# Performance work log

Measured on AMD Instinct MI355X. Metric: run time of the kernel, lower is better.

## Reference

```python
import jax, jax.numpy as jnp
import numpy as np
from jax import lax

K = 50            # n_segments in original SLIC call
ITERS = 10        # SLIC k-means iterations (skimage default max_num_iter=10)
COMPACTNESS = 10.0  # skimage SLIC default compactness


def _slic_weights(img):
    """SLIC-style superpixel segmentation of img [H,W,3] -> per-pixel weight 1/|segment|.

    Faithful to the module's use of skimage.slic: k-means in joint (color, xy)
    space with spatial coords scaled by compactness/S, S = sqrt(H*W/K),
    grid-initialized centers, then weight[p] = 1/count(segment[p]).
    """
    H, W, _ = img.shape
    N = H * W
    S = float(np.sqrt(N / K))
    ratio = COMPACTNESS / S
    yy, xx = jnp.meshgrid(jnp.arange(H, dtype=img.dtype),
                          jnp.arange(W, dtype=img.dtype), indexing='ij')
    feats = jnp.concatenate(
        [img.reshape(N, 3), (jnp.stack([yy, xx], -1).reshape(N, 2)) * ratio],
        axis=-1)  # [N,5]

    # grid-initialized centers (static shapes -> numpy at trace time)
    n = int(np.ceil(np.sqrt(K)))
    cy = ((np.arange(n) + 0.5) * H / n).astype(np.int64)
    cx = ((np.arange(n) + 0.5) * W / n).astype(np.int64)
    gy, gx = np.meshgrid(cy, cx, indexing='ij')
    init_idx = jnp.asarray((gy * W + gx).reshape(-1)[:K])
    centers0 = feats[init_idx]  # [K,5]

    f2 = jnp.sum(feats * feats, axis=-1)  # [N]

    def assign(centers):
        # squared distances via expansion: avoids [N,K,5] intermediate
        c2 = jnp.sum(centers * centers, axis=-1)            # [K]
        d = f2[:, None] + c2[None, :] - 2.0 * feats @ centers.T  # [N,K]
        return jnp.argmin(d, axis=1)

    def step(centers, _):
        lab = assign(centers)
        sums = jax.ops.segment_sum(feats, lab, num_segments=K)
        cnts = jax.ops.segment_sum(jnp.ones((N,), feats.dtype), lab, num_segments=K)
        new_centers = sums / jnp.maximum(cnts, 1.0)[:, None]
        return new_centers, None

    centers, _ = lax.scan(step, centers0, None, length=ITERS)
    lab = assign(centers)                                   # [N]
    cnts = jax.ops.segment_sum(jnp.ones((N,), feats.dtype), lab, num_segments=K)
    w = (1.0 / jnp.maximum(cnts, 1.0))[lab]                 # [N], 1/|segment|
    return w.reshape(H, W)


def setup_inputs() -> dict:
    key = jax.random.key(0)
    x = jax.random.uniform(key, (16, 3, 512, 512), dtype=jnp.float32)
    return {"x": x}


def reference(x):
    # per-pixel segment weights (computed from detached data in the original)
    w = lax.stop_gradient(jax.vmap(_slic_weights)(x.transpose(0, 2, 3, 1)))  # [B,H,W]
    xw = x * w[:, None, :, :]                    # broadcast over RGB channels
    mean_rgb = jnp.mean(xw, axis=(2, 3), keepdims=True)  # [B,3,1,1]
    mr = mean_rgb[:, 0:1]
    mg = mean_rgb[:, 1:2]
    mb = mean_rgb[:, 2:3]
    Drg = (mr - mg) ** 2
    Drb = (mr - mb) ** 2
    Dgb = (mb - mg) ** 2
    k = jnp.sqrt(Drg ** 2 + Drb ** 2 + Dgb ** 2)  # [B,1,1,1]
    return k
```

## Files before the change

### kernel.cpp

```cpp
#include <hip/hip_runtime.h>
#include <cmath>

#define K_SEG 50
#define ITERS 10
#define NPASS (ITERS + 1)
#define H_IMG 512
#define W_IMG 512
#define NPIX (H_IMG * W_IMG)
#define BATCH 16
#define SLOTS (K_SEG * 6)
#define TOTAL_SLOTS (NPASS * BATCH * SLOTS)


__global__ void zero_all(double* __restrict__ g) {
    int i = blockIdx.x * 256 + threadIdx.x;
    if (i < TOTAL_SLOTS) g[i] = 0.0;
}

__global__ void __launch_bounds__(256) assign_fused(
        const float* __restrict__ x, double* __restrict__ gsums,
        int it, float ratiof) {
    __shared__ float cen[K_SEG][6];
    __shared__ float cmax[K_SEG];
    __shared__ double part[K_SEG][6];
    __shared__ int klist4[4][52];
    __shared__ int ncand4[4];

    int t = threadIdx.x;
    int tx = blockIdx.x, ty = blockIdx.y, b = blockIdx.z;
    const float* xb = x + (size_t)b * 3 * NPIX;

    if (it == 0) {
        if (t < K_SEG) {
            int i = t >> 3, j = t & 7;
            int y = 32 + 64 * i, xc = 32 + 64 * j;
            int p = y * W_IMG + xc;
            float r = xb[p], g = xb[NPIX + p], bl = xb[2 * NPIX + p];
            float cfy = (float)y * ratiof, cfx = (float)xc * ratiof;
            cen[t][0]=r; cen[t][1]=g; cen[t][2]=bl; cen[t][3]=cfy; cen[t][4]=cfx;
            cen[t][5] = 0.5f * ((((r*r + g*g) + bl*bl) + cfy*cfy) + cfx*cfx);
            float m0 = fmaxf(r, 1.0f - r), m1 = fmaxf(g, 1.0f - g), m2 = fmaxf(bl, 1.0f - bl);
            cmax[t] = (m0*m0 + m1*m1) + m2*m2;
        }
    } else {
        const double* gp = gsums + ((size_t)(it - 1) * BATCH + b) * SLOTS;
        for (int i = t; i < SLOTS; i += 256) ((double*)part)[i] = gp[i];
        __syncthreads();
        if (t < K_SEG) {
            double cv = part[t][5];
            double denom = cv > 1.0 ? cv : 1.0;
            float c0 = (float)(part[t][0] / denom);
            float c1 = (float)(part[t][1] / denom);
            float c2v = (float)(part[t][2] / denom);
            float c3 = (float)(part[t][3] / denom);
            float c4 = (float)(part[t][4] / denom);
            cen[t][0]=c0; cen[t][1]=c1; cen[t][2]=c2v; cen[t][3]=c3; cen[t][4]=c4;
            cen[t][5] = 0.5f * ((((c0*c0 + c1*c1) + c2v*c2v) + c3*c3) + c4*c4);
            float m0 = fmaxf(c0, 1.0f - c0), m1 = fmaxf(c1, 1.0f - c1), m2 = fmaxf(c2v, 1.0f - c2v);
            cmax[t] = (m0*m0 + m1*m1) + m2*m2;
        }
    }
    __syncthreads();

    int wid = t >> 6;
    int lane = t & 63;
    {
        float Rmin = INFINITY, val = INFINITY;
        if (lane < K_SEG) {
            float cy = cen[lane][3], cxx = cen[lane][4];
            float y0 = (float)(ty * 64 + wid * 16) * ratiof;
            float y1 = (float)(ty * 64 + wid * 16 + 15) * ratiof;
            float x0 = (float)(tx * 64) * ratiof;
            float x1 = (float)(tx * 64 + 63) * ratiof;
            float dyn = fmaxf(fmaxf(y0 - cy, cy - y1), 0.0f);
            float dxn = fmaxf(fmaxf(x0 - cxx, cxx - x1), 0.0f);
            float dyf = fmaxf(cy - y0, y1 - cy);
            float dxf = fmaxf(cxx - x0, x1 - cxx);
            Rmin = dyn * dyn + dxn * dxn;
            val = (dyf * dyf + dxf * dxf) + cmax[lane];
        }
        float u = val;
        for (int off = 32; off; off >>= 1) u = fminf(u, __shfl_xor(u, off));
        bool cand = (lane < K_SEG) && (Rmin <= u + 0.25f);
        unsigned long long m = __ballot(cand);
        if (cand) {
            int pos = __popcll(m & ((1ull << lane) - 1ull));
            klist4[wid][pos] = lane;
        }
        if (lane == 0) ncand4[wid] = __popcll(m);
    }
    for (int i = t; i < SLOTS; i += 256) ((double*)part)[i] = 0.0;
    __syncthreads();
    int nc = ncand4[wid];

    int row = t >> 2;
    int colq = (t & 3) << 4;
    int gy = ty * 64 + row;
    int gx0 = tx * 64 + colq;
    float fy = (float)gy * ratiof;

    int runlab = -1;
    float sr = 0.0f, sg = 0.0f, sb = 0.0f, sfx = 0.0f;
    int rn = 0;
    for (int h = 0; h < 2; ++h) {
        int gx = gx0 + h * 8;
        size_t p = (size_t)gy * W_IMG + gx;
        float4 ra = *(const float4*)(xb + p);
        float4 rb4 = *(const float4*)(xb + p + 4);
        float4 ga = *(const float4*)(xb + NPIX + p);
        float4 gb4 = *(const float4*)(xb + NPIX + p + 4);
        float4 ba = *(const float4*)(xb + 2 * NPIX + p);
        float4 bb4 = *(const float4*)(xb + 2 * NPIX + p + 4);
        float rr[8] = {ra.x, ra.y, ra.z, ra.w, rb4.x, rb4.y, rb4.z, rb4.w};
        float gg[8] = {ga.x, ga.y, ga.z, ga.w, gb4.x, gb4.y, gb4.z, gb4.w};
        float bv[8] = {ba.x, ba.y, ba.z, ba.w, bb4.x, bb4.y, bb4.z, bb4.w};
        float fx8[8], best8[8];
        int lab8[8];
#pragma unroll
        for (int u2 = 0; u2 < 8; ++u2) {
            fx8[u2] = (float)(gx + u2) * ratiof;
            best8[u2] = INFINITY;
            lab8[u2] = 0;
        }
        for (int c = 0; c < nc; ++c) {
            int k = klist4[wid][c];
            float c0 = cen[k][0], c1 = cen[k][1], c2v = cen[k][2];
            float c3 = cen[k][3], c4 = cen[k][4], h2 = cen[k][5];
            float base = fmaf(fy, -c3, h2);
#pragma unroll
            for (int u2 = 0; u2 < 8; ++u2) {
                float s = fmaf(rr[u2], -c0, base);
                s = fmaf(gg[u2], -c1, s);
                s = fmaf(bv[u2], -c2v, s);
                s = fmaf(fx8[u2], -c4, s);
                if (s < best8[u2]) { best8[u2] = s; lab8[u2] = k; }
            }
        }
#pragma unroll
        for (int u2 = 0; u2 < 8; ++u2) {
            if (lab8[u2] != runlab) {
                if (rn > 0) {
                    double* pp = part[runlab];
                    unsafeAtomicAdd(&pp[0], (double)sr);
                    unsafeAtomicAdd(&pp[1], (double)sg);
                    unsafeAtomicAdd(&pp[2], (double)sb);
                    unsafeAtomicAdd(&pp[3], (double)fy * (double)rn);
                    unsafeAtomicAdd(&pp[4], (double)sfx);
                    unsafeAtomicAdd(&pp[5], (double)rn);
                }
                runlab = lab8[u2];
                sr = rr[u2]; sg = gg[u2]; sb = bv[u2]; sfx = fx8[u2]; rn = 1;
            } else {
                sr += rr[u2]; sg += gg[u2]; sb += bv[u2]; sfx += fx8[u2]; rn += 1;
            }
        }
    }
    if (rn > 0) {
        double* pp = part[runlab];
        unsafeAtomicAdd(&pp[0], (double)sr);
        unsafeAtomicAdd(&pp[1], (double)sg);
        unsafeAtomicAdd(&pp[2], (double)sb);
        unsafeAtomicAdd(&pp[3], (double)fy * (double)rn);
        unsafeAtomicAdd(&pp[4], (double)sfx);
        unsafeAtomicAdd(&pp[5], (double)rn);
    }
    __syncthreads();

    double* gp = gsums + ((size_t)it * BATCH + b) * SLOTS;
    for (int i = t; i < SLOTS; i += 256) {
        double v = ((double*)part)[i];
        if (v != 0.0) unsafeAtomicAdd(&gp[i], v);
    }
}

__global__ void finalize_kernel(const double* __restrict__ gsums, float* __restrict__ out) {
    int t = threadIdx.x;
    if (t < BATCH) {
        const double* gp = gsums + ((size_t)ITERS * BATCH + t) * SLOTS;
        double sr = 0.0, sg = 0.0, sb = 0.0;
        for (int k = 0; k < K_SEG; ++k) {
            const double* s = gp + k * 6;
            double cv = s[5];
            float cntf = (float)(cv > 1.0 ? cv : 1.0);
            float wf = 1.0f / cntf;
            sr += s[0] * (double)wf;
            sg += s[1] * (double)wf;
            sb += s[2] * (double)wf;
        }
        double mr = sr / (double)NPIX, mg = sg / (double)NPIX, mb = sb / (double)NPIX;
        double Drg = (mr - mg) * (mr - mg);
        double Drb = (mr - mb) * (mr - mb);
        double Dgb = (mb - mg) * (mb - mg);
        out[t] = (float)sqrt(Drg * Drg + Drb * Drb + Dgb * Dgb);
    }
}


__global__ void init_kernelF(const float* __restrict__ x, double* __restrict__ gsums,
                             float* __restrict__ centers, float* __restrict__ c2s,
                             float ratiof) {
    int b = blockIdx.x;
    int t = threadIdx.x;
    for (int i = t; i < SLOTS; i += blockDim.x) gsums[b * SLOTS + i] = 0.0;
    if (t < K_SEG) {
        int i = t >> 3, j = t & 7;
        int y = 32 + 64 * i, xc = 32 + 64 * j;
        const float* xb = x + (size_t)b * 3 * NPIX;
        int p = y * W_IMG + xc;
        float r = xb[p], g = xb[NPIX + p], bl = xb[2 * NPIX + p];
        float fyc = (float)y * ratiof, fxc = (float)xc * ratiof;
        float* c = centers + (b * K_SEG + t) * 5;
        c[0] = r; c[1] = g; c[2] = bl; c[3] = fyc; c[4] = fxc;
        c2s[b * K_SEG + t] = (((r * r + g * g) + bl * bl) + fyc * fyc) + fxc * fxc;
    }
}

__global__ void __launch_bounds__(128, 4) assign_kernelF(
        const float* __restrict__ x, double* __restrict__ gsums,
        const float* __restrict__ centers, const float* __restrict__ c2s,
        float ratiof) {
    __shared__ float cen[K_SEG][5];
    __shared__ float c2l[K_SEG];
    __shared__ double part[K_SEG][6];
    __shared__ int klist[K_SEG];
    __shared__ int ncand_s;

    int t = threadIdx.x;
    int tx = blockIdx.x, ty = blockIdx.y, b = blockIdx.z;

    const float* csrc = centers + b * K_SEG * 5;
    for (int i = t; i < K_SEG * 5; i += 128) ((float*)cen)[i] = csrc[i];
    for (int i = t; i < K_SEG; i += 128) c2l[i] = c2s[b * K_SEG + i];
    for (int i = t; i < SLOTS; i += 128) ((double*)part)[i] = 0.0;
    __syncthreads();

    if (t < 64) {
        int k = t;
        float R = INFINITY, val = INFINITY;
        if (k < K_SEG) {
            float cy = cen[k][3], cx = cen[k][4];
            float y0 = (float)(ty * 32) * ratiof;
            float y1 = (float)(ty * 32 + 31) * ratiof;
            float x0 = (float)(tx * 64) * ratiof;
            float x1 = (float)(tx * 64 + 63) * ratiof;
            float dyn = fmaxf(fmaxf(y0 - cy, cy - y1), 0.0f);
            float dxn = fmaxf(fmaxf(x0 - cx, cx - x1), 0.0f);
            float dyf = fmaxf(cy - y0, y1 - cy);
            float dxf = fmaxf(cx - x0, x1 - cx);
            R = dyn * dyn + dxn * dxn;
            val = (dyf * dyf + dxf * dxf) + 3.0f;
        }
        float u = val;
        for (int off = 32; off; off >>= 1) u = fminf(u, __shfl_xor(u, off));
        bool cand = (k < K_SEG) && (R <= u + 4.0f);
        unsigned long long m = __ballot(cand);
        if (cand) {
            int pos = __popcll(m & ((1ull << t) - 1ull));
            klist[pos] = k;
        }
        if (t == 0) ncand_s = __popcll(m);
    }
    __syncthreads();
    int ncand = ncand_s;

    int row = t >> 2;
    int colq = (t & 3) << 4;
    int gy = ty * 32 + row;
    int gx0 = tx * 64 + colq;
    const float* xb = x + (size_t)b * 3 * NPIX;
    float fy = (float)gy * ratiof;

    int runlab = -1;
    float sr = 0.0f, sg = 0.0f, sb = 0.0f, sfx = 0.0f;
    int rn = 0;

    for (int h = 0; h < 2; ++h) {
        int gx = gx0 + h * 8;
        size_t p = (size_t)gy * W_IMG + gx;
        float4 ra = *(const float4*)(xb + p);
        float4 rb4 = *(const float4*)(xb + p + 4);
        float4 ga = *(const float4*)(xb + NPIX + p);
        float4 gb4 = *(const float4*)(xb + NPIX + p + 4);
        float4 ba = *(const float4*)(xb + 2 * NPIX + p);
        float4 bb4 = *(const float4*)(xb + 2 * NPIX + p + 4);
        float rr[8] = {ra.x, ra.y, ra.z, ra.w, rb4.x, rb4.y, rb4.z, rb4.w};
        float gg[8] = {ga.x, ga.y, ga.z, ga.w, gb4.x, gb4.y, gb4.z, gb4.w};
        float bv[8] = {ba.x, ba.y, ba.z, ba.w, bb4.x, bb4.y, bb4.z, bb4.w};
        float fx8[8], f28[8], best8[8];
        int lab8[8];
#pragma unroll
        for (int u2 = 0; u2 < 8; ++u2) {
            fx8[u2] = (float)(gx + u2) * ratiof;
            f28[u2] = (((rr[u2] * rr[u2] + gg[u2] * gg[u2]) + bv[u2] * bv[u2]) + fy * fy) + fx8[u2] * fx8[u2];
            best8[u2] = INFINITY;
            lab8[u2] = 0;
        }
        for (int c = 0; c < ncand; ++c) {
            int k = klist[c];
            float c0 = cen[k][0], c1 = cen[k][1], c2v = cen[k][2], c3 = cen[k][3], c4 = cen[k][4];
            float c2k = c2l[k];
#pragma unroll
            for (int u2 = 0; u2 < 8; ++u2) {
                float dot = rr[u2] * c0 + gg[u2] * c1 + bv[u2] * c2v + fy * c3 + fx8[u2] * c4;
                float d = (f28[u2] + c2k) - 2.0f * dot;
                if (d < best8[u2]) { best8[u2] = d; lab8[u2] = k; }
            }
        }
#pragma unroll
        for (int u2 = 0; u2 < 8; ++u2) {
            if (lab8[u2] != runlab) {
                if (rn > 0) {
                    double* pp = part[runlab];
                    unsafeAtomicAdd(&pp[0], (double)sr);
                    unsafeAtomicAdd(&pp[1], (double)sg);
                    unsafeAtomicAdd(&pp[2], (double)sb);
                    unsafeAtomicAdd(&pp[3], (double)fy * (double)rn);
                    unsafeAtomicAdd(&pp[4], (double)sfx);
                    unsafeAtomicAdd(&pp[5], (double)rn);
                }
                runlab = lab8[u2];
                sr = rr[u2]; sg = gg[u2]; sb = bv[u2]; sfx = fx8[u2]; rn = 1;
            } else {
                sr += rr[u2]; sg += gg[u2]; sb += bv[u2]; sfx += fx8[u2]; rn += 1;
            }
        }
    }
    if (rn > 0) {
        double* pp = part[runlab];
        unsafeAtomicAdd(&pp[0], (double)sr);
        unsafeAtomicAdd(&pp[1], (double)sg);
        unsafeAtomicAdd(&pp[2], (double)sb);
        unsafeAtomicAdd(&pp[3], (double)fy * (double)rn);
        unsafeAtomicAdd(&pp[4], (double)sfx);
        unsafeAtomicAdd(&pp[5], (double)rn);
    }
    __syncthreads();
    for (int i = t; i < SLOTS; i += 128) {
        double v = ((double*)part)[i];
        if (v != 0.0) unsafeAtomicAdd(&gsums[b * SLOTS + i], v);
    }
}

__global__ void update_kernelF(double* __restrict__ gsums, float* __restrict__ centers,
                               float* __restrict__ c2s) {
    int b = blockIdx.x;
    int t = threadIdx.x;
    if (t < K_SEG) {
        double* s = gsums + (b * K_SEG + t) * 6;
        double cv = s[5];
        double denom = cv > 1.0 ? cv : 1.0;
        float c[5];
#pragma unroll
        for (int j = 0; j < 5; ++j) { c[j] = (float)(s[j] / denom); s[j] = 0.0; }
        s[5] = 0.0;
        float* cd = centers + (b * K_SEG + t) * 5;
#pragma unroll
        for (int j = 0; j < 5; ++j) cd[j] = c[j];
        c2s[b * K_SEG + t] = (((c[0] * c[0] + c[1] * c[1]) + c[2] * c[2]) + c[3] * c[3]) + c[4] * c[4];
    }
}

__global__ void finalize_kernelF(const double* __restrict__ gsums, float* __restrict__ out) {
    int t = threadIdx.x;
    if (t < BATCH) {
        double sr = 0.0, sg = 0.0, sb = 0.0;
        for (int k = 0; k < K_SEG; ++k) {
            const double* s = gsums + (t * K_SEG + k) * 6;
            double cv = s[5];
            float cntf = (float)(cv > 1.0 ? cv : 1.0);
            float wf = 1.0f / cntf;
            sr += s[0] * (double)wf;
            sg += s[1] * (double)wf;
            sb += s[2] * (double)wf;
        }
        double mr = sr / (double)NPIX, mg = sg / (double)NPIX, mb = sb / (double)NPIX;
        double Drg = (mr - mg) * (mr - mg);
        double Drb = (mr - mb) * (mr - mb);
        double Dgb = (mb - mg) * (mb - mg);
        out[t] = (float)sqrt(Drg * Drg + Drb * Drb + Dgb * Dgb);
    }
}

extern "C" void kernel_launch(void* const* d_in, const int* in_sizes, int n_in,
                              void* d_out, int out_size, void* d_ws, size_t ws_size,
                              hipStream_t stream) {
    const float* x = (const float*)d_in[0];
    float* out = (float*)d_out;
    char* ws = (char*)d_ws;

    double S = sqrt((double)NPIX / (double)K_SEG);
    float ratiof = (float)(10.0 / S);

    if (ws_size >= (size_t)TOTAL_SLOTS * sizeof(double)) {
        double* gsums = (double*)ws;
        zero_all<<<(TOTAL_SLOTS + 255) / 256, 256, 0, stream>>>(gsums);
        dim3 agrid(W_IMG / 64, H_IMG / 64, BATCH);
        for (int it = 0; it < NPASS; ++it)
            assign_fused<<<agrid, 256, 0, stream>>>(x, gsums, it, ratiof);
        finalize_kernel<<<1, 64, 0, stream>>>(gsums, out);
        return;
    }

    const size_t gbytes = (size_t)BATCH * SLOTS * sizeof(double);
    double* gsums = (double*)ws;
    float* centers = (float*)(ws + gbytes);
    float* c2s = (float*)(ws + gbytes + (size_t)BATCH * K_SEG * 5 * 4);

    init_kernelF<<<BATCH, 64, 0, stream>>>(x, gsums, centers, c2s, ratiof);
    dim3 agrid(W_IMG / 64, H_IMG / 32, BATCH);
    for (int it = 0; it < ITERS; ++it) {
        assign_kernelF<<<agrid, 128, 0, stream>>>(x, gsums, centers, c2s, ratiof);
        update_kernelF<<<BATCH, 64, 0, stream>>>(gsums, centers, c2s);
    }
    assign_kernelF<<<agrid, 128, 0, stream>>>(x, gsums, centers, c2s, ratiof);
    finalize_kernelF<<<1, 64, 0, stream>>>(gsums, out);
}
```

Before: 238.6 us.

## Aggregate final run sums per label across the wave before LDS atomics

```diff
diff --git a/kernel.cpp b/kernel.cpp
--- a/kernel.cpp
+++ b/kernel.cpp
@@ -49,11 +49,12 @@
         if (t < K_SEG) {
             double cv = part[t][5];
             double denom = cv > 1.0 ? cv : 1.0;
-            float c0 = (float)(part[t][0] / denom);
-            float c1 = (float)(part[t][1] / denom);
-            float c2v = (float)(part[t][2] / denom);
-            float c3 = (float)(part[t][3] / denom);
-            float c4 = (float)(part[t][4] / denom);
+            double rcp = 1.0 / denom;
+            float c0 = (float)(part[t][0] * rcp);
+            float c1 = (float)(part[t][1] * rcp);
+            float c2v = (float)(part[t][2] * rcp);
+            float c3 = (float)(part[t][3] * rcp);
+            float c4 = (float)(part[t][4] * rcp);
             cen[t][0]=c0; cen[t][1]=c1; cen[t][2]=c2v; cen[t][3]=c3; cen[t][4]=c4;
             cen[t][5] = 0.5f * ((((c0*c0 + c1*c1) + c2v*c2v) + c3*c3) + c4*c4);
             float m0 = fmaxf(c0, 1.0f - c0), m1 = fmaxf(c1, 1.0f - c1), m2 = fmaxf(c2v, 1.0f - c2v);
@@ -100,7 +101,7 @@
     float fy = (float)gy * ratiof;
 
     int runlab = -1;
-    float sr = 0.0f, sg = 0.0f, sb = 0.0f, sfx = 0.0f;
+    float sr = 0.0f, sg = 0.0f, sb = 0.0f, scol = 0.0f;
     int rn = 0;
     for (int h = 0; h < 2; ++h) {
         int gx = gx0 + h * 8;
@@ -144,31 +145,58 @@
                     unsafeAtomicAdd(&pp[0], (double)sr);
                     unsafeAtomicAdd(&pp[1], (double)sg);
                     unsafeAtomicAdd(&pp[2], (double)sb);
-                    unsafeAtomicAdd(&pp[3], (double)fy * (double)rn);
-                    unsafeAtomicAdd(&pp[4], (double)sfx);
+                    unsafeAtomicAdd(&pp[3], (double)((float)(gy * rn)));
+                    unsafeAtomicAdd(&pp[4], (double)scol);
                     unsafeAtomicAdd(&pp[5], (double)rn);
                 }
                 runlab = lab8[u2];
-                sr = rr[u2]; sg = gg[u2]; sb = bv[u2]; sfx = fx8[u2]; rn = 1;
+                sr = rr[u2]; sg = gg[u2]; sb = bv[u2]; scol = (float)(gx + u2); rn = 1;
             } else {
-                sr += rr[u2]; sg += gg[u2]; sb += bv[u2]; sfx += fx8[u2]; rn += 1;
-            }
-        }
-    }
-    if (rn > 0) {
-        double* pp = part[runlab];
-        unsafeAtomicAdd(&pp[0], (double)sr);
-        unsafeAtomicAdd(&pp[1], (double)sg);
-        unsafeAtomicAdd(&pp[2], (double)sb);
-        unsafeAtomicAdd(&pp[3], (double)fy * (double)rn);
-        unsafeAtomicAdd(&pp[4], (double)sfx);
-        unsafeAtomicAdd(&pp[5], (double)rn);
+                sr += rr[u2]; sg += gg[u2]; sb += bv[u2]; scol += (float)(gx + u2); rn += 1;
+            }
+        }
+    }
+
+    {
+        float fsr = sr, fsg = sg, fsb = sb, fscol = scol;
+        float fsrow = (float)(gy * rn);
+        float frn = (float)rn;
+        unsigned long long remaining = __ballot(true);
+        while (remaining) {
+            int leader = __ffsll((unsigned long long)remaining) - 1;
+            int labL = __shfl(runlab, leader);
+            bool in = (runlab == labL);
+            unsigned long long grp = __ballot(in);
+            float a0 = in ? fsr : 0.0f, a1 = in ? fsg : 0.0f, a2 = in ? fsb : 0.0f;
+            float a3 = in ? fsrow : 0.0f, a4 = in ? fscol : 0.0f, a5 = in ? frn : 0.0f;
+#pragma unroll
+            for (int off = 1; off < 64; off <<= 1) {
+                a0 += __shfl_xor(a0, off);
+                a1 += __shfl_xor(a1, off);
+                a2 += __shfl_xor(a2, off);
+                a3 += __shfl_xor(a3, off);
+                a4 += __shfl_xor(a4, off);
+                a5 += __shfl_xor(a5, off);
+            }
+            if (lane == leader) {
+                double* pp = part[labL];
+                unsafeAtomicAdd(&pp[0], (double)a0);
+                unsafeAtomicAdd(&pp[1], (double)a1);
+                unsafeAtomicAdd(&pp[2], (double)a2);
+                unsafeAtomicAdd(&pp[3], (double)a3);
+                unsafeAtomicAdd(&pp[4], (double)a4);
+                unsafeAtomicAdd(&pp[5], (double)a5);
+            }
+            remaining &= ~grp;
+        }
     }
     __syncthreads();
 
     double* gp = gsums + ((size_t)it * BATCH + b) * SLOTS;
     for (int i = t; i < SLOTS; i += 256) {
         double v = ((double*)part)[i];
+        int slot = i % 6;
+        if (slot == 3 || slot == 4) v *= (double)ratiof;
         if (v != 0.0) unsafeAtomicAdd(&gp[i], v);
     }
 }
```

Measured after the change: 213.7 us. 1.12x faster.
